# Kernel optimization log

Measured on AMD Instinct MI355X. Metric: run time of the kernel, lower is better.

Reference implementation:

```python
import jax, jax.numpy as jnp
import numpy as np

BODY_EDGES = [(0, 2), (0, 5), (2, 7), (5, 8), (11, 12), (0, 11), (0, 12), (7, 11), (8, 12), (11, 13), (13, 15), (12, 14), (14, 16), (11, 23), (12, 24), (23, 24), (11, 24), (12, 23)]
N_JOINTS = 33
N_FEAT = 52
HIDDEN = 128
BN_EPS = 1e-5


def _make_adj():
    a = np.eye(N_JOINTS, dtype=np.float32)
    for i, j in BODY_EDGES:
        a[i, j] = 1.0
        a[j, i] = 1.0
    deg = np.clip(a.sum(1), 1.0, None)
    d = deg ** -0.5
    return jnp.asarray(d[:, None] * a * d[None, :])


def setup_inputs() -> dict:
    key = jax.random.key(0)
    ks = iter(jax.random.split(key, 40))
    B, T = 64, 256
    def lin(k, i, o):
        return jax.random.normal(k, (i, o), jnp.float32) / np.sqrt(i)
    inp = {
        'x': jax.random.normal(next(ks), (B, T, N_JOINTS, N_FEAT), jnp.float32),
        'adj': _make_adj(),
        # layer 0: in 52 -> out 128 (has skip linear)
        'W0': lin(next(ks), N_FEAT, HIDDEN), 'b0': jax.random.normal(next(ks), (HIDDEN,)) * 0.02,
        'S0': lin(next(ks), N_FEAT, HIDDEN), 'sb0': jax.random.normal(next(ks), (HIDDEN,)) * 0.02,
        'g0': 1.0 + 0.1 * jax.random.normal(next(ks), (HIDDEN,)), 'be0': 0.1 * jax.random.normal(next(ks), (HIDDEN,)),
        'm0': 0.1 * jax.random.normal(next(ks), (HIDDEN,)), 'v0': 1.0 + 0.1 * jax.random.uniform(next(ks), (HIDDEN,)),
        # layers 1,2: 128 -> 128 (identity skip)
        'W1': lin(next(ks), HIDDEN, HIDDEN), 'b1': jax.random.normal(next(ks), (HIDDEN,)) * 0.02,
        'g1': 1.0 + 0.1 * jax.random.normal(next(ks), (HIDDEN,)), 'be1': 0.1 * jax.random.normal(next(ks), (HIDDEN,)),
        'm1': 0.1 * jax.random.normal(next(ks), (HIDDEN,)), 'v1': 1.0 + 0.1 * jax.random.uniform(next(ks), (HIDDEN,)),
        'W2': lin(next(ks), HIDDEN, HIDDEN), 'b2': jax.random.normal(next(ks), (HIDDEN,)) * 0.02,
        'g2': 1.0 + 0.1 * jax.random.normal(next(ks), (HIDDEN,)), 'be2': 0.1 * jax.random.normal(next(ks), (HIDDEN,)),
        'm2': 0.1 * jax.random.normal(next(ks), (HIDDEN,)), 'v2': 1.0 + 0.1 * jax.random.uniform(next(ks), (HIDDEN,)),
        # temporal attention MLP: 128 -> 128 -> 1
        'tW1': lin(next(ks), HIDDEN, HIDDEN), 'tb1': jax.random.normal(next(ks), (HIDDEN,)) * 0.02,
        'tW2': lin(next(ks), HIDDEN, 1), 'tb2': jax.random.normal(next(ks), (1,)) * 0.02,
    }
    return inp


def _gcn(h, adj, W, b, g, be, m, v, skip):
    # adjacency mix: [B*T, J, D_in]
    a = jnp.einsum('nm,bmd->bnd', adj, h)
    z = a @ W + b
    z = (z - m) * jax.lax.rsqrt(v + BN_EPS) * g + be  # eval-mode BatchNorm1d
    return jax.nn.gelu(z, approximate=False) + skip


def reference(x, adj, W0, b0, S0, sb0, g0, be0, m0, v0,
              W1, b1, g1, be1, m1, v1,
              W2, b2, g2, be2, m2, v2,
              tW1, tb1, tW2, tb2):
    B, T, J, Fd = x.shape
    h = x.reshape(B * T, J, Fd)
    h = _gcn(h, adj, W0, b0, g0, be0, m0, v0, h @ S0 + sb0)
    h = _gcn(h, adj, W1, b1, g1, be1, m1, v1, h)
    h = _gcn(h, adj, W2, b2, g2, be2, m2, v2, h)
    # dropout inactive (eval mode)
    xt = h.mean(axis=1).reshape(B, T, -1)                  # [B, T, H]
    score = jax.nn.gelu(xt @ tW1 + tb1, approximate=False) @ tW2 + tb2  # [B, T, 1]
    attn = jax.nn.softmax(score, axis=1)
    return (xt * attn).sum(axis=1)                         # [B, H]
```

## Files before the change

### kernel.cpp

```cpp
#include <hip/hip_runtime.h>
#include <hip/hip_bf16.h>
#include <math.h>


#define NJ 33
#define NF 52
#define NH 128
#define NT 256
#define NB 64
#define NSAMP (NB*NT)
#define SPB 2
#define NBLKS (NSAMP/SPB)
#define HSTR 136
#define PSTR 40

typedef unsigned short u16;
typedef _Float16 f16;
typedef f16   half8 __attribute__((ext_vector_type(8)));
typedef f16   h2    __attribute__((ext_vector_type(2)));
typedef float f32x4 __attribute__((ext_vector_type(4)));

#define HO_W0    0
#define HO_S0    8192
#define HO_W1    16384
#define HO_W2    32768
#define HO_TW1   49152
#define HO_ADJ32 65536
#define H_TOTAL  66560
#define FO_BASE  (H_TOTAL/2)
#define FO_A0    (FO_BASE+0)
#define FO_SB0   (FO_BASE+768)
#define FO_TB1   (FO_BASE+896)
#define FO_TW2   (FO_BASE+1024)
#define FO_XT    (FO_BASE+1152)
#define FO_SC    (FO_XT + NSAMP*NH)

__device__ __forceinline__ float bf2f(u16 u) { return __uint_as_float(((unsigned)u) << 16); }
__device__ __forceinline__ float ldv(const void* p, long i, int f) {
    float r;
    if (f) r = bf2f(((const u16*)p)[i]);
    else   r = ((const float*)p)[i];
    return r;
}
__device__ int detect_bf16(const void* p) {
    const u16* q = (const u16*)p;
    int nz = 0, ok = 0;
#pragma unroll
    for (int k = 0; k < 64; k++) {
        u16 u = q[k];
        if (u & 0x7FFF) {
            nz++;
            int e = (u >> 7) & 0xFF;
            ok += (e >= 0x40 && e <= 0xBF) ? 1 : 0;
        }
    }
    return (nz == 0) || (ok * 20 >= nz * 19);
}

__device__ __forceinline__ float gelu_t(float x) {
    float xc = fminf(fmaxf(x, -8.f), 8.f);
    float u  = xc * fmaf(xc * xc, 0.10294324f, 2.3022082f);
#if __has_builtin(__builtin_amdgcn_exp2f)
    float e  = __builtin_amdgcn_exp2f(u);
#else
    float e  = exp2f(u);
#endif
#if __has_builtin(__builtin_amdgcn_rcpf)
    float tt = (e - 1.f) * __builtin_amdgcn_rcpf(e + 1.f);
#else
    float tt = (e - 1.f) / (e + 1.f);
#endif
    float hx = 0.5f * x;
    return fmaf(hx, tt, hx);
}

#define MFMA16(a, b, c) __builtin_amdgcn_mfma_f32_16x16x32_f16(a, b, c, 0, 0, 0)

__global__ __launch_bounds__(256) void prep(
    const void* adj,
    const void* W0, const void* b0, const void* S0, const void* sb0,
    const void* g0, const void* be0, const void* m0, const void* v0,
    const void* W1, const void* b1, const void* g1, const void* be1, const void* m1, const void* v1,
    const void* W2, const void* b2, const void* g2, const void* be2, const void* m2, const void* v2,
    const void* tW1, const void* tb1, const void* tW2,
    void* ws)
{
    f16* H = (f16*)ws; float* F = (float*)ws;
    const int bi = blockIdx.x, t = threadIdx.x;
    if (bi == 0) {
        const int fW = detect_bf16(W0), fS = detect_bf16(S0);
        for (int i = t; i < NF * 128; i += 256) {
            int k = i >> 7, n = i & 127;
            H[HO_W0 + n * 64 + k] = (f16)ldv(W0, i, fW);
            H[HO_S0 + n * 64 + k] = (f16)ldv(S0, i, fS);
        }
        for (int i = t; i < 128 * 16; i += 256) {
            int n = i >> 4, k = 48 + (i & 15);
            if (k >= NF) { H[HO_W0 + n * 64 + k] = (f16)0.f; H[HO_S0 + n * 64 + k] = (f16)0.f; }
        }
    } else if (bi == 1) {
        const int f = detect_bf16(W1);
        for (int i = t; i < 128 * 128; i += 256) {
            int k = i >> 7, n = i & 127;
            H[HO_W1 + n * 128 + k] = (f16)ldv(W1, i, f);
        }
    } else if (bi == 2) {
        const int f = detect_bf16(W2);
        for (int i = t; i < 128 * 128; i += 256) {
            int k = i >> 7, n = i & 127;
            H[HO_W2 + n * 128 + k] = (f16)ldv(W2, i, f);
        }
    } else if (bi == 3) {
        const int f = detect_bf16(tW1);
        for (int i = t; i < 128 * 128; i += 256) {
            int k = i >> 7, n = i & 127;
            H[HO_TW1 + n * 128 + k] = (f16)ldv(tW1, i, f);
        }
    } else {
        if (t < 128) {
            int c = t;
            {
                float g = ldv(g0,c,detect_bf16(g0)), be = ldv(be0,c,detect_bf16(be0));
                float m = ldv(m0,c,detect_bf16(m0)), v = ldv(v0,c,detect_bf16(v0));
                float b = ldv(b0,c,detect_bf16(b0));
                float A = g * rsqrtf(v + 1e-5f);
                F[FO_A0 + 0*256 + c] = A; F[FO_A0 + 0*256 + 128 + c] = (b - m)*A + be;
            }
            {
                float g = ldv(g1,c,detect_bf16(g1)), be = ldv(be1,c,detect_bf16(be1));
                float m = ldv(m1,c,detect_bf16(m1)), v = ldv(v1,c,detect_bf16(v1));
                float b = ldv(b1,c,detect_bf16(b1));
                float A = g * rsqrtf(v + 1e-5f);
                F[FO_A0 + 1*256 + c] = A; F[FO_A0 + 1*256 + 128 + c] = (b - m)*A + be;
            }
            {
                float g = ldv(g2,c,detect_bf16(g2)), be = ldv(be2,c,detect_bf16(be2));
                float m = ldv(m2,c,detect_bf16(m2)), v = ldv(v2,c,detect_bf16(v2));
                float b = ldv(b2,c,detect_bf16(b2));
                float A = g * rsqrtf(v + 1e-5f);
                F[FO_A0 + 2*256 + c] = A; F[FO_A0 + 2*256 + 128 + c] = (b - m)*A + be;
            }
            F[FO_SB0 + c] = ldv(sb0, c, detect_bf16(sb0));
            F[FO_TB1 + c] = ldv(tb1, c, detect_bf16(tb1));
            F[FO_TW2 + c] = ldv(tW2, c, detect_bf16(tW2));
        }
        const int fA = detect_bf16(adj);
        for (int i = t; i < 1024; i += 256) {
            int r = i >> 5, c = i & 31;
            float v = (r < 25 && c < 25) ? ldv(adj, (long)r*NJ + c, fA) : 0.f;
            H[HO_ADJ32 + i] = (f16)v;
        }
    }
}

#define PTWRITE(ACC)                                                            \
    _Pragma("unroll")                                                           \
    for (int mt = 0; mt < 6; mt++) {                                            \
        if (mt != 2 && mt != 5) {                                               \
            const int sW = (mt >= 3) ? 1 : 0;                                   \
            const int jb = (mt - 3*sW) * 16;                                    \
            _Pragma("unroll")                                                   \
            for (int nt = 0; nt < 2; nt++) {                                    \
                f16* pp = Pt + sW*5120 + (nt ? c1 : c0)*PSTR;                   \
                _Pragma("unroll")                                               \
                for (int r2 = 0; r2 < 4; r2 += 2) {                             \
                    int j0 = jb + q*4 + r2;                                     \
                    if (j0 + 1 < 25) {                                          \
                        h2 v2w = { (f16)ACC[mt][nt][r2], (f16)ACC[mt][nt][r2+1] }; \
                        *(h2*)(pp + j0) = v2w;                                  \
                    } else if (j0 < 25) {                                       \
                        pp[j0] = (f16)ACC[mt][nt][r2];                          \
                    }                                                           \
                }                                                               \
            }                                                                   \
        }                                                                       \
    }

#define ADJEPI(L, ISL0, WRHB) {                                                 \
    half8 afadj0 = *(const half8*)(HW + HO_ADJ32 + ml*32 + q*8);                \
    half8 afadj1 = *(const half8*)(HW + HO_ADJ32 + (16+ml)*32 + q*8);           \
    f32x4 zac[2][2][2];                                                         \
    _Pragma("unroll")                                                           \
    for (int sW = 0; sW < 2; sW++) {                                            \
        _Pragma("unroll")                                                       \
        for (int nt = 0; nt < 2; nt++) {                                        \
            half8 bz = *(const half8*)(Pt + sW*5120 + (nt?c1:c0)*PSTR + q*8);   \
            zac[sW][0][nt] = MFMA16(afadj0, bz, z4);                            \
            zac[sW][1][nt] = MFMA16(afadj1, bz, z4);                            \
        }                                                                       \
    }                                                                           \
    _Pragma("unroll")                                                           \
    for (int nt = 0; nt < 2; nt++) {                                            \
        const int cc = nt ? c1 : c0;                                            \
        const float Av = rA[L][nt], Dv = rD[L][nt];                             \
        const float sbv = nt ? sb0b : sb0a;                                     \
        _Pragma("unroll")                                                       \
        for (int sW = 0; sW < 2; sW++) {                                        \
            _Pragma("unroll")                                                   \
            for (int m2 = 0; m2 < 2; m2++) {                                    \
                _Pragma("unroll")                                               \
                for (int r4 = 0; r4 < 4; r4++) {                                \
                    float zv = (m2 == 0) ? zac[sW][0][nt][r4]                   \
                             : (jlt[r4] ? zac[sW][1][nt][r4]                    \
                                        : acc[3*sW+1][nt][r4]);                 \
                    float hold = (ISL0) ? (acs[3*sW+m2][nt][r4] + sbv)          \
                                        : hz[sW][m2][nt][r4];                   \
                    float hnew = gelu_t(fmaf(zv, Av, Dv)) + hold;               \
                    hz[sW][m2][nt][r4] = hnew;                                  \
                    if (WRHB)                                                   \
                        hb[(sW*48 + m2*16 + q*4 + r4)*HSTR + cc] = (f16)hnew;   \
                }                                                               \
            }                                                                   \
            {                                                                   \
                float zv = acc[3*sW+2][nt][0];                                  \
                float hold = (ISL0) ? (acs[3*sW+2][nt][0] + sbv)                \
                                    : h32[sW][nt];                              \
                float hnew = gelu_t(fmaf(zv, Av, Dv)) + hold;                   \
                h32[sW][nt] = (q == 0) ? hnew : 0.f;                            \
                if (WRHB && q == 0)                                             \
                    hb[(sW*48 + 32)*HSTR + cc] = (f16)hnew;                     \
            }                                                                   \
        }                                                                       \
    }                                                                           \
}

#define GEMM128(WOFF)                                                           \
    {                                                                           \
        half8 bf[2][4];                                                         \
        _Pragma("unroll")                                                       \
        for (int nt = 0; nt < 2; nt++)                                          \
            _Pragma("unroll")                                                   \
            for (int ks = 0; ks < 4; ks++)                                      \
                bf[nt][ks] = *(const half8*)(HW + (WOFF) + (nt?c1:c0)*128 + ks*32 + q*8); \
        _Pragma("unroll")                                                       \
        for (int mt = 0; mt < 6; mt++) { acc[mt][0] = z4; acc[mt][1] = z4; }    \
        _Pragma("unroll")                                                       \
        for (int mt = 0; mt < 6; mt++) {                                        \
            const int m = mt*16 + ml;                                           \
            _Pragma("unroll")                                                   \
            for (int ks = 0; ks < 4; ks++) {                                    \
                half8 af = *(const half8*)(hb + m*HSTR + ks*32 + q*8);          \
                acc[mt][0] = MFMA16(af, bf[0][ks], acc[mt][0]);                 \
                acc[mt][1] = MFMA16(af, bf[1][ks], acc[mt][1]);                 \
            }                                                                   \
        }                                                                       \
    }

__global__ __launch_bounds__(256) void gcn_mfma(const void* __restrict__ x,
                                                void* __restrict__ ws)
{
    const f16* HW = (const f16*)ws;
    float* F = (float*)ws;
    float* xt_g = F + FO_XT;
    float* sc_g = F + FO_SC;

    __shared__ __align__(16) f16 hb[96 * HSTR];
    __shared__ __align__(16) f16 Pt[2 * 128 * PSTR];
    __shared__ float sTB1[128], sTW2[128];
    __shared__ float rbuf4[4];
    __shared__ int sfx;
    float* xtb = (float*)Pt;

    const int t = threadIdx.x, lane = t & 63, wv = t >> 6;
    const int q = lane >> 4, ml = lane & 15;
    const int n0 = wv * 32;
    const int c0 = n0 + ml, c1 = n0 + 16 + ml;
    const f32x4 z4 = {0.f, 0.f, 0.f, 0.f};
    const bool jlt[4] = { q <= 2, q <= 1, q <= 1, q <= 1 };

    if (t == 0) sfx = detect_bf16(x);
    if (t < 128) { sTB1[t] = F[FO_TB1 + t]; sTW2[t] = F[FO_TW2 + t]; }
    for (int i = t; i < 2048; i += 256) {
        int sW = i >> 10, n = (i >> 3) & 127, k = 24 + (i & 7);
        Pt[sW*5120 + n*PSTR + k] = (f16)0.f;
    }

    float rA[3][2], rD[3][2];
#pragma unroll
    for (int L = 0; L < 3; L++) {
        rA[L][0] = F[FO_A0 + L*256 + c0];        rA[L][1] = F[FO_A0 + L*256 + c1];
        rD[L][0] = F[FO_A0 + L*256 + 128 + c0];  rD[L][1] = F[FO_A0 + L*256 + 128 + c1];
    }
    const float sb0a = F[FO_SB0 + c0], sb0b = F[FO_SB0 + c1];
    __syncthreads();

    {
        const int fX = sfx;
        const long xb = (long)blockIdx.x * (SPB * NJ * NF);
#pragma unroll 1
        for (int it = 0; it < 3; it++) {
            int g = t + it * 256;
            if (g < 66 * 8) {
                int r = g >> 3, blk = g & 7;
                int fr = (r < 33) ? r : r + 15;
                long rb = xb + (long)r * NF;
                half8 o;
#pragma unroll
                for (int i = 0; i < 8; i++) {
                    int cx = blk * 8 + i;
                    o[i] = (f16)(cx < NF ? ldv(x, rb + cx, fX) : 0.f);
                }
                *(half8*)(hb + fr * HSTR + blk * 8) = o;
            }
        }
    }
    __syncthreads();

    f32x4 acc[6][2];
    f32x4 acs[6][2];
    float hz[2][2][2][4];
    float h32[2][2];

    {
        half8 bw[2][2], bs[2][2];
#pragma unroll
        for (int nt = 0; nt < 2; nt++) {
            int n = nt ? c1 : c0;
#pragma unroll
            for (int ks = 0; ks < 2; ks++) {
                bw[nt][ks] = *(const half8*)(HW + HO_W0 + n*64 + ks*32 + q*8);
                bs[nt][ks] = *(const half8*)(HW + HO_S0 + n*64 + ks*32 + q*8);
            }
        }
#pragma unroll
        for (int mt = 0; mt < 6; mt++) { acc[mt][0]=z4; acc[mt][1]=z4; acs[mt][0]=z4; acs[mt][1]=z4; }
#pragma unroll
        for (int mt = 0; mt < 6; mt++) {
            const int m = mt*16 + ml;
            half8 a0 = *(const half8*)(hb + m*HSTR + q*8);
            half8 a1 = *(const half8*)(hb + m*HSTR + 32 + q*8);
            acc[mt][0] = MFMA16(a0, bw[0][0], acc[mt][0]);
            acc[mt][0] = MFMA16(a1, bw[0][1], acc[mt][0]);
            acc[mt][1] = MFMA16(a0, bw[1][0], acc[mt][1]);
            acc[mt][1] = MFMA16(a1, bw[1][1], acc[mt][1]);
            acs[mt][0] = MFMA16(a0, bs[0][0], acs[mt][0]);
            acs[mt][0] = MFMA16(a1, bs[0][1], acs[mt][0]);
            acs[mt][1] = MFMA16(a0, bs[1][0], acs[mt][1]);
            acs[mt][1] = MFMA16(a1, bs[1][1], acs[mt][1]);
        }
        __syncthreads();
        PTWRITE(acc)
        ADJEPI(0, 1, 1)
        __syncthreads();
    }

    GEMM128(HO_W1)
    __syncthreads();
    PTWRITE(acc)
    ADJEPI(1, 0, 1)
    __syncthreads();

    GEMM128(HO_W2)
    __syncthreads();
    PTWRITE(acc)
    ADJEPI(2, 0, 0)
    __syncthreads();

#pragma unroll
    for (int sW = 0; sW < 2; sW++)
#pragma unroll
        for (int nt = 0; nt < 2; nt++) {
            float s = h32[sW][nt];
#pragma unroll
            for (int m2 = 0; m2 < 2; m2++)
#pragma unroll
                for (int r4 = 0; r4 < 4; r4++) s += hz[sW][m2][nt][r4];
            s += __shfl_xor(s, 16, 64);
            s += __shfl_xor(s, 32, 64);
            float xtc = s * (1.0f / 33.0f);
            if (q == 0) {
                int cc = nt ? c1 : c0;
                xtb[sW * 128 + cc] = xtc;
                xt_g[((long)blockIdx.x * SPB + sW) * NH + cc] = xtc;
            }
        }
    __syncthreads();

    {
        const int sW = t >> 7, c = t & 127;
        float u = 0.f;
#pragma unroll
        for (int kk = 0; kk < 16; kk++) {
            half8 wv8 = *(const half8*)(HW + HO_TW1 + c*128 + kk*8);
#pragma unroll
            for (int i = 0; i < 8; i++)
                u = fmaf(xtb[sW*128 + kk*8 + i], (float)wv8[i], u);
        }
        float r = gelu_t(u + sTB1[c]) * sTW2[c];
#pragma unroll
        for (int off = 32; off > 0; off >>= 1) r += __shfl_xor(r, off, 64);
        if (lane == 0) rbuf4[wv] = r;
        __syncthreads();
        if (t == 0) {
            sc_g[blockIdx.x * SPB + 0] = rbuf4[0] + rbuf4[1];
            sc_g[blockIdx.x * SPB + 1] = rbuf4[2] + rbuf4[3];
        }
    }
}

__global__ __launch_bounds__(256) void attn_pool(
    const void* __restrict__ x,
    const float* __restrict__ xt_ws, const float* __restrict__ score_ws,
    void* __restrict__ out)
{
    __shared__ float ew[NT];
    __shared__ float red[8];
    __shared__ float pb[256];
    __shared__ int sfx2;
    const int t = threadIdx.x, lane = t & 63, wv = t >> 6;
    const int b = blockIdx.x >> 2, qr = blockIdx.x & 3;

    if (t == 0) sfx2 = detect_bf16(x);
    float sv = score_ws[b * NT + t];
    float m = sv;
#pragma unroll
    for (int off = 32; off > 0; off >>= 1) m = fmaxf(m, __shfl_xor(m, off, 64));
    if (lane == 0) red[wv] = m;
    __syncthreads();
    float mx = fmaxf(fmaxf(red[0], red[1]), fmaxf(red[2], red[3]));
    float e = __expf(sv - mx);
    ew[t] = e;
    float d = e;
#pragma unroll
    for (int off = 32; off > 0; off >>= 1) d += __shfl_xor(d, off, 64);
    if (lane == 0) red[4 + wv] = d;
    __syncthreads();
    float den = red[4] + red[5] + red[6] + red[7];

    const int cl = t & 31, ch = t >> 5;
    const int c = qr * 32 + cl;
    float a = 0.f;
#pragma unroll 4
    for (int i = ch * 32; i < ch * 32 + 32; i++)
        a = fmaf(ew[i], xt_ws[((long)b * NT + i) * NH + c], a);
    pb[t] = a;
    __syncthreads();
    if (t < 128) pb[t] += pb[t + 128];
    __syncthreads();
    if (t < 64) pb[t] += pb[t + 64];
    __syncthreads();
    if (t < 32) {
        float r = (pb[t] + pb[t + 32]) / den;
        if (sfx2) ((__hip_bfloat16*)out)[b * NH + qr * 32 + t] = __float2bfloat16(r);
        else      ((float*)out)[b * NH + qr * 32 + t] = r;
    }
}

extern "C" void kernel_launch(void* const* d_in, const int* in_sizes, int n_in,
                              void* d_out, int out_size, void* d_ws, size_t ws_size,
                              hipStream_t stream) {
    prep<<<5, 256, 0, stream>>>(
        d_in[1],
        d_in[2], d_in[3], d_in[4], d_in[5],
        d_in[6], d_in[7], d_in[8], d_in[9],
        d_in[10], d_in[11], d_in[12], d_in[13], d_in[14], d_in[15],
        d_in[16], d_in[17], d_in[18], d_in[19], d_in[20], d_in[21],
        d_in[22], d_in[23], d_in[24],
        d_ws);
    gcn_mfma<<<NBLKS, 256, 0, stream>>>(d_in[0], d_ws);
    float* F = (float*)d_ws;
    attn_pool<<<NB * 4, 256, 0, stream>>>(d_in[0], F + FO_XT, F + FO_SC, d_out);
}
```

Measured before the change: 608.4 us.

## Repack two samples into five M-tiles and vectorize fp32 input loads

Joint rows of the two samples per block are rearranged so that the first 32 joints of each sample fill four 16-row tiles and both samples' joint 32 share a fifth tile. This cuts the MFMA M-tiles per GEMM from 6 to 5 and shrinks the shared hidden buffer. The fp32 input path now loads with float4 instead of per-element converts. The layer-0 skip initialization moves out of the epilogue so the skip accumulators can be released early, and the adjacency fragments are hoisted out of the epilogue macro. The extra indexing complexity adds risk around the mixed joint-32 tile.

```diff
diff --git a/kernel.cpp b/kernel.cpp
--- a/kernel.cpp
+++ b/kernel.cpp
@@ -155,70 +155,60 @@
 
 #define PTWRITE(ACC)                                                            \
     _Pragma("unroll")                                                           \
-    for (int mt = 0; mt < 6; mt++) {                                            \
-        if (mt != 2 && mt != 5) {                                               \
-            const int sW = (mt >= 3) ? 1 : 0;                                   \
-            const int jb = (mt - 3*sW) * 16;                                    \
+    for (int mt = 0; mt < 4; mt++) {                                            \
+        const int fF = mt >> 1;                                                 \
+        const int jb = (mt & 1) * 16;                                           \
+        _Pragma("unroll")                                                       \
+        for (int nt = 0; nt < 2; nt++) {                                        \
+            f16* pp = Pt + (fF*128 + (nt ? c1 : c0))*PSTR;                      \
             _Pragma("unroll")                                                   \
-            for (int nt = 0; nt < 2; nt++) {                                    \
-                f16* pp = Pt + sW*5120 + (nt ? c1 : c0)*PSTR;                   \
-                _Pragma("unroll")                                               \
-                for (int r2 = 0; r2 < 4; r2 += 2) {                             \
-                    int j0 = jb + q*4 + r2;                                     \
-                    if (j0 + 1 < 25) {                                          \
-                        h2 v2w = { (f16)ACC[mt][nt][r2], (f16)ACC[mt][nt][r2+1] }; \
-                        *(h2*)(pp + j0) = v2w;                                  \
-                    } else if (j0 < 25) {                                       \
-                        pp[j0] = (f16)ACC[mt][nt][r2];                          \
-                    }                                                           \
+            for (int r2 = 0; r2 < 4; r2 += 2) {                                 \
+                int j0 = jb + q*4 + r2;                                         \
+                if (j0 + 1 < 25) {                                              \
+                    h2 v2w = { (f16)ACC[mt][nt][r2], (f16)ACC[mt][nt][r2+1] };  \
+                    *(h2*)(pp + j0) = v2w;                                      \
+                } else if (j0 < 25) {                                           \
+                    pp[j0] = (f16)ACC[mt][nt][r2];                              \
                 }                                                               \
             }                                                                   \
         }                                                                       \
     }
 
-#define ADJEPI(L, ISL0, WRHB) {                                                 \
-    half8 afadj0 = *(const half8*)(HW + HO_ADJ32 + ml*32 + q*8);                \
-    half8 afadj1 = *(const half8*)(HW + HO_ADJ32 + (16+ml)*32 + q*8);           \
+#define ADJEPI(L, WRHB) {                                                       \
     f32x4 zac[2][2][2];                                                         \
     _Pragma("unroll")                                                           \
-    for (int sW = 0; sW < 2; sW++) {                                            \
+    for (int fF = 0; fF < 2; fF++) {                                            \
         _Pragma("unroll")                                                       \
         for (int nt = 0; nt < 2; nt++) {                                        \
-            half8 bz = *(const half8*)(Pt + sW*5120 + (nt?c1:c0)*PSTR + q*8);   \
-            zac[sW][0][nt] = MFMA16(afadj0, bz, z4);                            \
-            zac[sW][1][nt] = MFMA16(afadj1, bz, z4);                            \
+            half8 bz = *(const half8*)(Pt + (fF*128 + (nt?c1:c0))*PSTR + q*8);  \
+            zac[fF][0][nt] = MFMA16(afadj0, bz, z4);                            \
+            zac[fF][1][nt] = MFMA16(afadj1, bz, z4);                            \
         }                                                                       \
     }                                                                           \
     _Pragma("unroll")                                                           \
     for (int nt = 0; nt < 2; nt++) {                                            \
         const int cc = nt ? c1 : c0;                                            \
         const float Av = rA[L][nt], Dv = rD[L][nt];                             \
-        const float sbv = nt ? sb0b : sb0a;                                     \
-        _Pragma("unroll")                                                       \
-        for (int sW = 0; sW < 2; sW++) {                                        \
+        _Pragma("unroll")                                                       \
+        for (int fF = 0; fF < 2; fF++) {                                        \
             _Pragma("unroll")                                                   \
             for (int m2 = 0; m2 < 2; m2++) {                                    \
                 _Pragma("unroll")                                               \
                 for (int r4 = 0; r4 < 4; r4++) {                                \
-                    float zv = (m2 == 0) ? zac[sW][0][nt][r4]                   \
-                             : (jlt[r4] ? zac[sW][1][nt][r4]                    \
-                                        : acc[3*sW+1][nt][r4]);                 \
-                    float hold = (ISL0) ? (acs[3*sW+m2][nt][r4] + sbv)          \
-                                        : hz[sW][m2][nt][r4];                   \
-                    float hnew = gelu_t(fmaf(zv, Av, Dv)) + hold;               \
-                    hz[sW][m2][nt][r4] = hnew;                                  \
+                    float zv = (m2 == 0) ? zac[fF][0][nt][r4]                   \
+                             : (jlt[r4] ? zac[fF][1][nt][r4]                    \
+                                        : acc[2*fF+1][nt][r4]);                 \
+                    float hnew = gelu_t(fmaf(zv, Av, Dv)) + hz[fF][m2][nt][r4]; \
+                    hz[fF][m2][nt][r4] = hnew;                                  \
                     if (WRHB)                                                   \
-                        hb[(sW*48 + m2*16 + q*4 + r4)*HSTR + cc] = (f16)hnew;   \
+                        hb[((2*fF+m2)*16 + q*4 + r4)*HSTR + cc] = (f16)hnew;    \
                 }                                                               \
             }                                                                   \
             {                                                                   \
-                float zv = acc[3*sW+2][nt][0];                                  \
-                float hold = (ISL0) ? (acs[3*sW+2][nt][0] + sbv)                \
-                                    : h32[sW][nt];                              \
-                float hnew = gelu_t(fmaf(zv, Av, Dv)) + hold;                   \
-                h32[sW][nt] = (q == 0) ? hnew : 0.f;                            \
+                float hnew = gelu_t(fmaf(acc[4][nt][fF], Av, Dv)) + h32[fF][nt];\
+                h32[fF][nt] = (q == 0) ? hnew : 0.f;                            \
                 if (WRHB && q == 0)                                             \
-                    hb[(sW*48 + 32)*HSTR + cc] = (f16)hnew;                     \
+                    hb[(64 + fF)*HSTR + cc] = (f16)hnew;                        \
             }                                                                   \
         }                                                                       \
     }                                                                           \
@@ -233,9 +223,9 @@
             for (int ks = 0; ks < 4; ks++)                                      \
                 bf[nt][ks] = *(const half8*)(HW + (WOFF) + (nt?c1:c0)*128 + ks*32 + q*8); \
         _Pragma("unroll")                                                       \
-        for (int mt = 0; mt < 6; mt++) { acc[mt][0] = z4; acc[mt][1] = z4; }    \
-        _Pragma("unroll")                                                       \
-        for (int mt = 0; mt < 6; mt++) {                                        \
+        for (int mt = 0; mt < 5; mt++) { acc[mt][0] = z4; acc[mt][1] = z4; }    \
+        _Pragma("unroll")                                                       \
+        for (int mt = 0; mt < 5; mt++) {                                        \
             const int m = mt*16 + ml;                                           \
             _Pragma("unroll")                                                   \
             for (int ks = 0; ks < 4; ks++) {                                    \
@@ -254,9 +244,8 @@
     float* xt_g = F + FO_XT;
     float* sc_g = F + FO_SC;
 
-    __shared__ __align__(16) f16 hb[96 * HSTR];
+    __shared__ __align__(16) f16 hb[80 * HSTR];
     __shared__ __align__(16) f16 Pt[2 * 128 * PSTR];
-    __shared__ float sTB1[128], sTW2[128];
     __shared__ float rbuf4[4];
     __shared__ int sfx;
     float* xtb = (float*)Pt;
@@ -267,12 +256,13 @@
     const int c0 = n0 + ml, c1 = n0 + 16 + ml;
     const f32x4 z4 = {0.f, 0.f, 0.f, 0.f};
     const bool jlt[4] = { q <= 2, q <= 1, q <= 1, q <= 1 };
+    const half8 zero8 = {(f16)0.f,(f16)0.f,(f16)0.f,(f16)0.f,(f16)0.f,(f16)0.f,(f16)0.f,(f16)0.f};
 
     if (t == 0) sfx = detect_bf16(x);
-    if (t < 128) { sTB1[t] = F[FO_TB1 + t]; sTW2[t] = F[FO_TW2 + t]; }
-    for (int i = t; i < 2048; i += 256) {
-        int sW = i >> 10, n = (i >> 3) & 127, k = 24 + (i & 7);
-        Pt[sW*5120 + n*PSTR + k] = (f16)0.f;
+#pragma unroll
+    for (int i = t; i < 512; i += 256) {
+        int fF = i >> 8, rem = i & 255, n = rem >> 1, ch = rem & 1;
+        *(half8*)(Pt + (fF*128 + n)*PSTR + 24 + ch*8) = zero8;
     }
 
     float rA[3][2], rD[3][2];
@@ -282,6 +272,8 @@
         rD[L][0] = F[FO_A0 + L*256 + 128 + c0];  rD[L][1] = F[FO_A0 + L*256 + 128 + c1];
     }
     const float sb0a = F[FO_SB0 + c0], sb0b = F[FO_SB0 + c1];
+    half8 afadj0 = *(const half8*)(HW + HO_ADJ32 + ml*32 + q*8);
+    half8 afadj1 = *(const half8*)(HW + HO_ADJ32 + (16+ml)*32 + q*8);
     __syncthreads();
 
     {
@@ -292,13 +284,29 @@
             int g = t + it * 256;
             if (g < 66 * 8) {
                 int r = g >> 3, blk = g & 7;
-                int fr = (r < 33) ? r : r + 15;
-                long rb = xb + (long)r * NF;
+                int fF = (r >= 33) ? 1 : 0;
+                int j = r - 33 * fF;
+                int fr = (j < 32) ? (fF * 32 + j) : (64 + fF);
                 half8 o;
-#pragma unroll
-                for (int i = 0; i < 8; i++) {
-                    int cx = blk * 8 + i;
-                    o[i] = (f16)(cx < NF ? ldv(x, rb + cx, fX) : 0.f);
+                if (!fX) {
+                    const float* base = (const float*)x + xb + (long)r * NF + blk * 8;
+                    if (blk < 6) {
+                        float4 v0 = *(const float4*)base;
+                        float4 v1 = *(const float4*)(base + 4);
+                        o[0]=(f16)v0.x; o[1]=(f16)v0.y; o[2]=(f16)v0.z; o[3]=(f16)v0.w;
+                        o[4]=(f16)v1.x; o[5]=(f16)v1.y; o[6]=(f16)v1.z; o[7]=(f16)v1.w;
+                    } else if (blk == 6) {
+                        float4 v0 = *(const float4*)base;
+                        o = zero8;
+                        o[0]=(f16)v0.x; o[1]=(f16)v0.y; o[2]=(f16)v0.z; o[3]=(f16)v0.w;
+                    } else o = zero8;
+                } else {
+                    long rb = xb + (long)r * NF;
+#pragma unroll
+                    for (int i = 0; i < 8; i++) {
+                        int cx = blk * 8 + i;
+                        o[i] = (f16)(cx < NF ? bf2f(((const u16*)x)[rb + cx]) : 0.f);
+                    }
                 }
                 *(half8*)(hb + fr * HSTR + blk * 8) = o;
             }
@@ -306,8 +314,7 @@
     }
     __syncthreads();
 
-    f32x4 acc[6][2];
-    f32x4 acs[6][2];
+    f32x4 acc[5][2];
     float hz[2][2][2][4];
     float h32[2][2];
 
@@ -322,10 +329,11 @@
                 bs[nt][ks] = *(const half8*)(HW + HO_S0 + n*64 + ks*32 + q*8);
             }
         }
-#pragma unroll
-        for (int mt = 0; mt < 6; mt++) { acc[mt][0]=z4; acc[mt][1]=z4; acs[mt][0]=z4; acs[mt][1]=z4; }
-#pragma unroll
-        for (int mt = 0; mt < 6; mt++) {
+        f32x4 acs[5][2];
+#pragma unroll
+        for (int mt = 0; mt < 5; mt++) { acc[mt][0]=z4; acc[mt][1]=z4; acs[mt][0]=z4; acs[mt][1]=z4; }
+#pragma unroll
+        for (int mt = 0; mt < 5; mt++) {
             const int m = mt*16 + ml;
             half8 a0 = *(const half8*)(hb + m*HSTR + q*8);
             half8 a1 = *(const half8*)(hb + m*HSTR + 32 + q*8);
@@ -340,53 +348,67 @@
         }
         __syncthreads();
         PTWRITE(acc)
-        ADJEPI(0, 1, 1)
+#pragma unroll
+        for (int fF = 0; fF < 2; fF++)
+#pragma unroll
+            for (int m2 = 0; m2 < 2; m2++)
+#pragma unroll
+                for (int nt = 0; nt < 2; nt++)
+#pragma unroll
+                    for (int r4 = 0; r4 < 4; r4++)
+                        hz[fF][m2][nt][r4] = acs[2*fF+m2][nt][r4] + (nt ? sb0b : sb0a);
+#pragma unroll
+        for (int fF = 0; fF < 2; fF++)
+#pragma unroll
+            for (int nt = 0; nt < 2; nt++)
+                h32[fF][nt] = (q == 0) ? (acs[4][nt][fF] + (nt ? sb0b : sb0a)) : 0.f;
+        ADJEPI(0, 1)
         __syncthreads();
     }
 
     GEMM128(HO_W1)
     __syncthreads();
     PTWRITE(acc)
-    ADJEPI(1, 0, 1)
+    ADJEPI(1, 1)
     __syncthreads();
 
     GEMM128(HO_W2)
     __syncthreads();
     PTWRITE(acc)
-    ADJEPI(2, 0, 0)
-    __syncthreads();
-
-#pragma unroll
-    for (int sW = 0; sW < 2; sW++)
+    ADJEPI(2, 0)
+    __syncthreads();
+
+#pragma unroll
+    for (int fF = 0; fF < 2; fF++)
 #pragma unroll
         for (int nt = 0; nt < 2; nt++) {
-            float s = h32[sW][nt];
+            float s = h32[fF][nt];
 #pragma unroll
             for (int m2 = 0; m2 < 2; m2++)
 #pragma unroll
-                for (int r4 = 0; r4 < 4; r4++) s += hz[sW][m2][nt][r4];
+                for (int r4 = 0; r4 < 4; r4++) s += hz[fF][m2][nt][r4];
             s += __shfl_xor(s, 16, 64);
             s += __shfl_xor(s, 32, 64);
             float xtc = s * (1.0f / 33.0f);
             if (q == 0) {
                 int cc = nt ? c1 : c0;
-                xtb[sW * 128 + cc] = xtc;
-                xt_g[((long)blockIdx.x * SPB + sW) * NH + cc] = xtc;
+                xtb[fF * 128 + cc] = xtc;
+                xt_g[((long)blockIdx.x * SPB + fF) * NH + cc] = xtc;
             }
         }
     __syncthreads();
 
     {
-        const int sW = t >> 7, c = t & 127;
+        const int fF = t >> 7, c = t & 127;
         float u = 0.f;
 #pragma unroll
         for (int kk = 0; kk < 16; kk++) {
             half8 wv8 = *(const half8*)(HW + HO_TW1 + c*128 + kk*8);
 #pragma unroll
             for (int i = 0; i < 8; i++)
-                u = fmaf(xtb[sW*128 + kk*8 + i], (float)wv8[i], u);
-        }
-        float r = gelu_t(u + sTB1[c]) * sTW2[c];
+                u = fmaf(xtb[fF*128 + kk*8 + i], (float)wv8[i], u);
+        }
+        float r = gelu_t(u + F[FO_TB1 + c]) * F[FO_TW2 + c];
 #pragma unroll
         for (int off = 32; off > 0; off >>= 1) r += __shfl_xor(r, off, 64);
         if (lane == 0) rbuf4[wv] = r;
```

Result: faster. 576.9 us (-5.2%).
